# Kernel optimization log

Hardware: AMD Instinct MI355X
Metric: run time of the kernel (lower is better)

The kernel has to match this reference:

```python
import jax, jax.numpy as jnp
import numpy as np
from functools import partial

# norse LIFAdEx default parameters
DT = 0.001
TAU_SYN_INV = 1.0 / 5e-3   # 200.0
TAU_MEM_INV = 1.0 / 1e-2   # 100.0
TAU_ADA_INV = 2.0
ADAPT_CURRENT = 4.0
ADAPT_SPIKE = 0.02
DELTA_T = 0.5
V_LEAK = 0.0
V_TH = 1.0
V_RESET = 0.0
ALPHA = 100.0              # superspike surrogate sharpness
TAU_FILTER_INV = 223.1435511314


@jax.custom_vjp
def superspike(x):
    # forward: heaviside; backward: superspike surrogate grad
    return (x > 0).astype(x.dtype)

def _ss_fwd(x):
    return superspike(x), x

def _ss_bwd(x, g):
    return (g / (ALPHA * jnp.abs(x) + 1.0) ** 2,)

superspike.defvjp(_ss_fwd, _ss_bwd)


def lif_adex_recurrent(x, W_in, W_rec):
    """x: (T,B,F) -> spikes (T,B,H). norse lif_adex_step semantics."""
    T, B, _ = x.shape
    H = W_rec.shape[0]
    # precompute feed-forward input current for all steps: (T,B,H)
    i_in = jnp.einsum('tbf,hf->tbh', x, W_in)

    def step(carry, ic):
        z, v, i, a = carry
        dv = DT * TAU_MEM_INV * ((V_LEAK - v)
                                 + DELTA_T * jnp.exp((v - V_TH) / DELTA_T)
                                 + i - a)
        v_dec = v + dv
        i_dec = i - DT * TAU_SYN_INV * i
        a_dec = a + DT * TAU_ADA_INV * (ADAPT_CURRENT * (v - V_LEAK) - a)
        z_new = superspike(v_dec - V_TH)
        v_new = (1.0 - z_new) * v_dec + z_new * V_RESET
        i_new = i_dec + ic + z @ W_rec.T
        a_new = a_dec + z_new * ADAPT_SPIKE
        return (z_new, v_new, i_new, a_new), z_new

    z0 = jnp.zeros((B, H), x.dtype)
    init = (z0, z0, z0, z0)
    _, spikes = jax.lax.scan(step, init, i_in)
    return spikes


def exp_filter(spikes, W_out, b_out):
    """Linear readout + exponential low-pass filter over time."""
    y = jnp.einsum('tbh,oh->tbo', spikes, W_out) + b_out  # (T,B,O)
    k = DT * TAU_FILTER_INV

    def step(o_prev, y_t):
        o = o_prev + k * (y_t - o_prev)
        return o, o

    o0 = y[0]
    _, rest = jax.lax.scan(step, o0, y[1:])
    return jnp.concatenate([o0[None], rest], axis=0)


def setup_inputs() -> dict:
    key = jax.random.key(0)
    kx, k1, k2, k3, k4 = jax.random.split(key, 5)
    T, B, F, H, O = 500, 128, 128, 512, 32
    x = jax.random.normal(kx, (T, B, F), dtype=jnp.float32)
    W_in = jax.random.normal(k1, (H, F), dtype=jnp.float32) * np.sqrt(2.0 / F)
    W_rec = jax.random.normal(k2, (H, H), dtype=jnp.float32) * np.sqrt(2.0 / H)
    W_out = jax.random.normal(k3, (O, H), dtype=jnp.float32) * np.sqrt(1.0 / H)
    b_out = jax.random.normal(k4, (O,), dtype=jnp.float32) * 0.01
    return {'x': x, 'W_in': W_in, 'W_rec': W_rec, 'W_out': W_out, 'b_out': b_out}


def reference(x, W_in, W_rec, W_out, b_out):
    spikes = lif_adex_recurrent(x, W_in, W_rec)
    return exp_filter(spikes, W_out, b_out)
```

## Files before the change

### kernel.cpp

```cpp
#include <hip/hip_runtime.h>
#include <hip/hip_bf16.h>
#include <cstdint>
#include <cstddef>

#define T_STEPS 500
#define BATCH   128
#define FDIM    128
#define HDIM    512
#define ODIM    32
#define M_ROWS  (T_STEPS * BATCH)
#define ZOFF    (512u << 11)

__device__ __forceinline__ float bfbits2f(unsigned short u) {
    union { unsigned int i; float f; } c; c.i = ((unsigned int)u) << 16; return c.f;
}

__global__ void detect_kernel(const unsigned short* __restrict__ xw, int* __restrict__ flag) {
    __shared__ int cnt;
    if (threadIdx.x == 0) cnt = 0;
    __syncthreads();
    unsigned short w = xw[threadIdx.x * 2];
    int e = (w >> 7) & 0xFF;
    if (e >= 170) atomicAdd(&cnt, 1);
    __syncthreads();
    if (threadIdx.x == 0) *flag = (cnt >= 8) ? 1 : 0;
}

__global__ void prep_kernel(const void* __restrict__ Wrec,
                            const void* __restrict__ Wout,
                            const void* __restrict__ bout,
                            const void* __restrict__ Win,
                            const int* __restrict__ flag,
                            float* __restrict__ WrecT,
                            float* __restrict__ WoutT,
                            float* __restrict__ WinT,
                            float* __restrict__ bout32) {
    const int fp32 = *flag;
    int idx = blockIdx.x * blockDim.x + threadIdx.x;
    if (idx < HDIM * HDIM) {
        int h  = idx / HDIM;
        int hp = idx % HDIM;
        float v = fp32 ? ((const float*)Wrec)[idx]
                       : bfbits2f(((const unsigned short*)Wrec)[idx]);
        WrecT[hp * HDIM + h] = v;
    }
    if (idx < HDIM) WrecT[HDIM * HDIM + idx] = 0.f;
    if (idx < ODIM * HDIM) {
        int o = idx / HDIM;
        int h = idx % HDIM;
        float v = fp32 ? ((const float*)Wout)[idx]
                       : bfbits2f(((const unsigned short*)Wout)[idx]);
        WoutT[h * ODIM + o] = v;
    }
    if (idx < HDIM * FDIM) {
        int h = idx / FDIM;
        int f = idx % FDIM;
        float v = fp32 ? ((const float*)Win)[idx]
                       : bfbits2f(((const unsigned short*)Win)[idx]);
        WinT[f * HDIM + h] = v;
    }
    if (idx < ODIM) {
        bout32[idx] = fp32 ? ((const float*)bout)[idx]
                           : bfbits2f(((const unsigned short*)bout)[idx]);
    }
}

__global__ __launch_bounds__(256) void iin_gemm(const void* __restrict__ x,
                                                const float* __restrict__ WinT,
                                                const int* __restrict__ flag,
                                                float* __restrict__ iin) {
    const int fp32 = *flag;
    const int tid  = threadIdx.x;
    const int m0   = blockIdx.x * 32;

    __shared__ float xs[32][FDIM];

    for (int i = tid; i < 32 * FDIM; i += 256) {
        size_t g = (size_t)m0 * FDIM + i;
        xs[0][i] = fp32 ? ((const float*)x)[g]
                        : bfbits2f(((const unsigned short*)x)[g]);
    }
    __syncthreads();

    float acc[32][2];
#pragma unroll
    for (int m = 0; m < 32; ++m) { acc[m][0] = 0.f; acc[m][1] = 0.f; }

#pragma unroll 4
    for (int k = 0; k < FDIM; ++k) {
        float w0 = WinT[(size_t)k * HDIM + tid];
        float w1 = WinT[(size_t)k * HDIM + 256 + tid];
#pragma unroll
        for (int m = 0; m < 32; ++m) {
            float xv = xs[m][k];
            acc[m][0] += xv * w0;
            acc[m][1] += xv * w1;
        }
    }

#pragma unroll
    for (int m = 0; m < 32; ++m) {
        iin[(size_t)(m0 + m) * HDIM + tid]       = acc[m][0];
        iin[(size_t)(m0 + m) * HDIM + 256 + tid] = acc[m][1];
    }
}

__global__ __launch_bounds__(1024) void scan_kernel(const float* __restrict__ iin,
                                                    const float* __restrict__ WrecT,
                                                    unsigned long long* __restrict__ masksG) {
    const int b    = blockIdx.x;
    const int tid  = threadIdx.x;
    const int h    = tid & (HDIM - 1);
    const int p    = tid >> 9;
    const int lane = tid & 63;
    const int wv   = tid >> 6;

    __shared__ unsigned long long wmask[8];
    __shared__ float part[2][HDIM];
    __shared__ alignas(16) unsigned int slAe[288], slAo[288];
    __shared__ alignas(16) unsigned int slBe[288], slBo[288];
    unsigned int *slOe = slAe, *slOo = slAo;
    unsigned int *slNe = slBe, *slNo = slBo;

    const float kDvC  = 0.1f;
    const float kSyn  = 0.2f;
    const float kAda  = 0.002f;

    float v = 0.f, cur = 0.f, a = 0.f;
    int   cnt = 0;
    const char* WB = (const char*)(WrecT + h);

    for (int t = 0; t < T_STEPS; ++t) {
        float ic = iin[((size_t)t * BATCH + b) * HDIM + h];

        float s = (0.0f - v) + 0.5f * expf((v - 1.0f) * 2.0f);
        s = s + cur;
        s = s - a;
        float v_dec = v + kDvC * s;
        float i_dec = cur - kSyn * cur;
        float a_dec = a + kAda * (4.0f * v - a);
        bool  zk    = (v_dec - 1.0f) > 0.0f;

        unsigned long long m = __ballot(zk);
        if (lane == 0 && wv < 8) {
            wmask[wv] = m;
            masksG[((size_t)t * BATCH + b) * 8 + wv] = m;
        }

        v = zk ? 0.0f : v_dec;
        a = zk ? (a_dec + 0.02f) : a_dec;

        float rsum = 0.f;
        {
            const unsigned int* sl = p ? slOo : slOe;
            const int n  = p ? (cnt >> 1) : ((cnt + 1) >> 1);
            const int ng = (n + 15) >> 4;
            float b0[16], b1[16];
            auto ld16 = [&](int g, float* d) {
                const uint4* q = (const uint4*)(sl + (g << 4));
                uint4 i0 = q[0], i1 = q[1], i2 = q[2], i3 = q[3];
                d[0]  = *(const float*)(WB + i0.x);
                d[1]  = *(const float*)(WB + i0.y);
                d[2]  = *(const float*)(WB + i0.z);
                d[3]  = *(const float*)(WB + i0.w);
                d[4]  = *(const float*)(WB + i1.x);
                d[5]  = *(const float*)(WB + i1.y);
                d[6]  = *(const float*)(WB + i1.z);
                d[7]  = *(const float*)(WB + i1.w);
                d[8]  = *(const float*)(WB + i2.x);
                d[9]  = *(const float*)(WB + i2.y);
                d[10] = *(const float*)(WB + i2.z);
                d[11] = *(const float*)(WB + i2.w);
                d[12] = *(const float*)(WB + i3.x);
                d[13] = *(const float*)(WB + i3.y);
                d[14] = *(const float*)(WB + i3.z);
                d[15] = *(const float*)(WB + i3.w);
            };
            int g = 0;
            if (ng > 0) ld16(0, b0);
            while (g + 2 <= ng) {
                ld16(g + 1, b1);
#pragma unroll
                for (int u = 0; u < 16; ++u) rsum += b0[u];
                if (g + 2 < ng) ld16(g + 2, b0);
#pragma unroll
                for (int u = 0; u < 16; ++u) rsum += b1[u];
                g += 2;
            }
            if (g < ng) {
#pragma unroll
                for (int u = 0; u < 16; ++u) rsum += b0[u];
            }
        }
        part[p][h] = rsum;

        __syncthreads();

        float rec = part[0][h] + part[1][h];
        cur = (i_dec + ic) + rec;

        int total = 0, off = 0;
        const int wv7 = wv & 7;
#pragma unroll
        for (int w = 0; w < 8; ++w) {
            int pc = __popcll(wmask[w]);
            if (w < wv7) off += pc;
            total += pc;
        }
        off += __popcll(m & ((1ull << lane) - 1ull));
        if (zk && p == 0) {
            unsigned int hoff = (unsigned int)h << 11;
            if (off & 1) slNo[off >> 1] = hoff;
            else         slNe[off >> 1] = hoff;
        }
        {
            int ne = (total + 1) >> 1, no = total >> 1;
            int neP = (ne + 15) & ~15, noP = (no + 15) & ~15;
            if (tid < neP - ne) slNe[ne + tid] = ZOFF;
            if (tid < noP - no) slNo[no + tid] = ZOFF;
        }
        cnt = total;

        __syncthreads();

        unsigned int* tp;
        tp = slOe; slOe = slNe; slNe = tp;
        tp = slOo; slOo = slNo; slNo = tp;
    }
}

__global__ __launch_bounds__(256) void y_kernel(const unsigned long long* __restrict__ masks,
                                                const float* __restrict__ WoutT,
                                                const float* __restrict__ bout,
                                                float* __restrict__ y) {
    const int tid = threadIdx.x;
    const int p   = blockIdx.x * 8 + (tid >> 5);
    const int o   = tid & 31;
    const unsigned long long* mp = masks + (size_t)p * 8;
    float acc = 0.f;
#pragma unroll
    for (int w = 0; w < 8; ++w) {
        unsigned long long m = mp[w];
        const float* Wb = WoutT + (size_t)w * 64 * ODIM + o;
        while (m) {
            int j = __builtin_ctzll(m);
            acc += Wb[j * ODIM];
            m &= m - 1;
        }
    }
    y[(size_t)p * ODIM + o] = acc + bout[o];
}

__global__ __launch_bounds__(64) void filter_kernel(const float* __restrict__ y,
                                                    const int* __restrict__ flag,
                                                    void* __restrict__ out) {
    const int p = blockIdx.x * 64 + threadIdx.x;
    const int fp32o = *flag;
    const float kf = 0.2231435511314f;
    float c0[10], c1[10];
#pragma unroll
    for (int u = 0; u < 10; ++u) c0[u] = y[(size_t)u * (BATCH * ODIM) + p];
    float o_state = 0.f;
    for (int base = 0; base < T_STEPS; base += 10) {
        if (base + 10 < T_STEPS) {
#pragma unroll
            for (int u = 0; u < 10; ++u)
                c1[u] = y[(size_t)(base + 10 + u) * (BATCH * ODIM) + p];
        }
#pragma unroll
        for (int u = 0; u < 10; ++u) {
            int t = base + u;
            float yt = c0[u];
            o_state = (t == 0) ? yt : (o_state + kf * (yt - o_state));
            size_t oi = (size_t)t * (BATCH * ODIM) + p;
            if (fp32o) ((float*)out)[oi] = o_state;
            else       ((__hip_bfloat16*)out)[oi] = __float2bfloat16(o_state);
        }
#pragma unroll
        for (int u = 0; u < 10; ++u) c0[u] = c1[u];
    }
}

extern "C" void kernel_launch(void* const* d_in, const int* in_sizes, int n_in,
                              void* d_out, int out_size, void* d_ws, size_t ws_size,
                              hipStream_t stream) {
    const void* x = d_in[0]; const void* Win = d_in[1]; const void* Wrec = d_in[2];
    const void* Wout = d_in[3]; const void* bout = d_in[4];
    for (int i = 0; i < n_in; ++i) {
        switch (in_sizes[i]) {
            case 8192000: x    = d_in[i]; break;
            case 65536:   Win  = d_in[i]; break;
            case 262144:  Wrec = d_in[i]; break;
            case 16384:   Wout = d_in[i]; break;
            case 32:      bout = d_in[i]; break;
            default: break;
        }
    }

    const size_t OFF_FLAG  = 0;
    const size_t OFF_BOUT  = 256;
    const size_t OFF_WOUTT = 512;
    const size_t OFF_WRECT = 66048;
    const size_t OFF_WINT  = 1116672;
    const size_t OFF_MASK  = 1378816;
    const size_t OFF_IIN   = 5474816;
    const size_t OFF_Y     = OFF_IIN;
    const size_t REQUIRED  = OFF_IIN + (size_t)M_ROWS * HDIM * 4;
    if (ws_size < REQUIRED) return;

    char* ws = (char*)d_ws;
    int*    flag   = (int*)(ws + OFF_FLAG);
    float*  bout32 = (float*)(ws + OFF_BOUT);
    float*  WoutT  = (float*)(ws + OFF_WOUTT);
    float*  WrecT  = (float*)(ws + OFF_WRECT);
    float*  WinT   = (float*)(ws + OFF_WINT);
    unsigned long long* masks = (unsigned long long*)(ws + OFF_MASK);
    float*  iin    = (float*)(ws + OFF_IIN);
    float*  y      = (float*)(ws + OFF_Y);

    hipLaunchKernelGGL(detect_kernel, dim3(1), dim3(256), 0, stream,
                       (const unsigned short*)x, flag);
    hipLaunchKernelGGL(prep_kernel, dim3((HDIM * HDIM + 255) / 256), dim3(256), 0, stream,
                       Wrec, Wout, bout, Win, flag, WrecT, WoutT, WinT, bout32);
    hipLaunchKernelGGL(iin_gemm, dim3(M_ROWS / 32), dim3(256), 0, stream,
                       x, WinT, flag, iin);
    hipLaunchKernelGGL(scan_kernel, dim3(BATCH), dim3(1024), 0, stream,
                       iin, WrecT, masks);
    hipLaunchKernelGGL(y_kernel, dim3(M_ROWS / 8), dim3(256), 0, stream,
                       masks, WoutT, bout32, y);
    hipLaunchKernelGGL(filter_kernel, dim3((BATCH * ODIM) / 64), dim3(64), 0, stream,
                       y, flag, d_out);
}
```

Baseline: 995.4 us.

## Repartition recurrent spike gather into 8 slices with float4 weight-row loads

```diff
diff --git a/kernel.cpp b/kernel.cpp
--- a/kernel.cpp
+++ b/kernel.cpp
@@ -110,17 +110,19 @@
                                                     unsigned long long* __restrict__ masksG) {
     const int b    = blockIdx.x;
     const int tid  = threadIdx.x;
-    const int h    = tid & (HDIM - 1);
-    const int p    = tid >> 9;
+    const int q    = tid & 127;
+    const int p    = tid >> 7;
     const int lane = tid & 63;
     const int wv   = tid >> 6;
+    const bool st  = tid < HDIM;
+    const int h    = tid;
 
     __shared__ unsigned long long wmask[8];
-    __shared__ float part[2][HDIM];
-    __shared__ alignas(16) unsigned int slAe[288], slAo[288];
-    __shared__ alignas(16) unsigned int slBe[288], slBo[288];
-    unsigned int *slOe = slAe, *slOo = slAo;
-    unsigned int *slNe = slBe, *slNo = slBo;
+    __shared__ float4 part[8][128];
+    __shared__ alignas(16) unsigned int slA[8][68];
+    __shared__ alignas(16) unsigned int slB[8][68];
+    unsigned int (*slO)[68] = slA;
+    unsigned int (*slN)[68] = slB;
 
     const float kDvC  = 0.1f;
     const float kSyn  = 0.2f;
@@ -128,104 +130,95 @@
 
     float v = 0.f, cur = 0.f, a = 0.f;
     int   cnt = 0;
-    const char* WB = (const char*)(WrecT + h);
+    const char* WQ = (const char*)WrecT + q * 16;
 
     for (int t = 0; t < T_STEPS; ++t) {
-        float ic = iin[((size_t)t * BATCH + b) * HDIM + h];
-
-        float s = (0.0f - v) + 0.5f * expf((v - 1.0f) * 2.0f);
-        s = s + cur;
-        s = s - a;
-        float v_dec = v + kDvC * s;
-        float i_dec = cur - kSyn * cur;
-        float a_dec = a + kAda * (4.0f * v - a);
-        bool  zk    = (v_dec - 1.0f) > 0.0f;
-
-        unsigned long long m = __ballot(zk);
-        if (lane == 0 && wv < 8) {
-            wmask[wv] = m;
-            masksG[((size_t)t * BATCH + b) * 8 + wv] = m;
-        }
-
-        v = zk ? 0.0f : v_dec;
-        a = zk ? (a_dec + 0.02f) : a_dec;
-
-        float rsum = 0.f;
+        float ic = 0.f, i_dec = 0.f;
+        bool  zk = false;
+        unsigned long long m = 0;
+
+        if (st) {
+            ic = iin[((size_t)t * BATCH + b) * HDIM + h];
+            float s = (0.0f - v) + 0.5f * expf((v - 1.0f) * 2.0f);
+            s = s + cur;
+            s = s - a;
+            float v_dec = v + kDvC * s;
+            i_dec = cur - kSyn * cur;
+            float a_dec = a + kAda * (4.0f * v - a);
+            zk = (v_dec - 1.0f) > 0.0f;
+
+            m = __ballot(zk);
+            if (lane == 0) {
+                wmask[wv] = m;
+                masksG[((size_t)t * BATCH + b) * 8 + wv] = m;
+            }
+            v = zk ? 0.0f : v_dec;
+            a = zk ? (a_dec + 0.02f) : a_dec;
+        }
+
+        float4 rs = {0.f, 0.f, 0.f, 0.f};
         {
-            const unsigned int* sl = p ? slOo : slOe;
-            const int n  = p ? (cnt >> 1) : ((cnt + 1) >> 1);
-            const int ng = (n + 15) >> 4;
-            float b0[16], b1[16];
-            auto ld16 = [&](int g, float* d) {
-                const uint4* q = (const uint4*)(sl + (g << 4));
-                uint4 i0 = q[0], i1 = q[1], i2 = q[2], i3 = q[3];
-                d[0]  = *(const float*)(WB + i0.x);
-                d[1]  = *(const float*)(WB + i0.y);
-                d[2]  = *(const float*)(WB + i0.z);
-                d[3]  = *(const float*)(WB + i0.w);
-                d[4]  = *(const float*)(WB + i1.x);
-                d[5]  = *(const float*)(WB + i1.y);
-                d[6]  = *(const float*)(WB + i1.z);
-                d[7]  = *(const float*)(WB + i1.w);
-                d[8]  = *(const float*)(WB + i2.x);
-                d[9]  = *(const float*)(WB + i2.y);
-                d[10] = *(const float*)(WB + i2.z);
-                d[11] = *(const float*)(WB + i2.w);
-                d[12] = *(const float*)(WB + i3.x);
-                d[13] = *(const float*)(WB + i3.y);
-                d[14] = *(const float*)(WB + i3.z);
-                d[15] = *(const float*)(WB + i3.w);
+            const int n  = (cnt + 7 - p) >> 3;
+            const int ng = (n + 3) >> 2;
+            float4 b0[4], b1[4];
+            auto ld4 = [&](int g, float4* d) {
+                uint4 i0 = *(const uint4*)&slO[p][g << 2];
+                d[0] = *(const float4*)(WQ + i0.x);
+                d[1] = *(const float4*)(WQ + i0.y);
+                d[2] = *(const float4*)(WQ + i0.z);
+                d[3] = *(const float4*)(WQ + i0.w);
+            };
+            auto acc4 = [&](const float4* d) {
+#pragma unroll
+                for (int u = 0; u < 4; ++u) {
+                    rs.x += d[u].x; rs.y += d[u].y; rs.z += d[u].z; rs.w += d[u].w;
+                }
             };
             int g = 0;
-            if (ng > 0) ld16(0, b0);
+            if (ng > 0) ld4(0, b0);
             while (g + 2 <= ng) {
-                ld16(g + 1, b1);
-#pragma unroll
-                for (int u = 0; u < 16; ++u) rsum += b0[u];
-                if (g + 2 < ng) ld16(g + 2, b0);
-#pragma unroll
-                for (int u = 0; u < 16; ++u) rsum += b1[u];
+                ld4(g + 1, b1);
+                acc4(b0);
+                if (g + 2 < ng) ld4(g + 2, b0);
+                acc4(b1);
                 g += 2;
             }
-            if (g < ng) {
-#pragma unroll
-                for (int u = 0; u < 16; ++u) rsum += b0[u];
+            if (g < ng) acc4(b0);
+        }
+        part[p][q] = rs;
+
+        __syncthreads();
+
+        int total = 0;
+#pragma unroll
+        for (int w = 0; w < 8; ++w) total += __popcll(wmask[w]);
+
+        if (st) {
+            float rec = 0.f;
+#pragma unroll
+            for (int pp = 0; pp < 8; ++pp)
+                rec += ((const float*)&part[pp][h >> 2])[h & 3];
+            cur = (i_dec + ic) + rec;
+
+            if (zk) {
+                int off = __popcll(m & ((1ull << lane) - 1ull));
+#pragma unroll
+                for (int w = 0; w < 8; ++w)
+                    if (w < wv) off += __popcll(wmask[w]);
+                slN[off & 7][off >> 3] = (unsigned int)h << 11;
             }
-        }
-        part[p][h] = rsum;
+        } else if (tid < HDIM + 32) {
+            int s  = (tid - HDIM) >> 2;
+            int k  = (tid - HDIM) & 3;
+            int ne = (total + 7 - s) >> 3;
+            int padc = (4 - (ne & 3)) & 3;
+            if (k < padc) slN[s][ne + k] = ZOFF;
+        }
+        cnt = total;
 
         __syncthreads();
 
-        float rec = part[0][h] + part[1][h];
-        cur = (i_dec + ic) + rec;
-
-        int total = 0, off = 0;
-        const int wv7 = wv & 7;
-#pragma unroll
-        for (int w = 0; w < 8; ++w) {
-            int pc = __popcll(wmask[w]);
-            if (w < wv7) off += pc;
-            total += pc;
-        }
-        off += __popcll(m & ((1ull << lane) - 1ull));
-        if (zk && p == 0) {
-            unsigned int hoff = (unsigned int)h << 11;
-            if (off & 1) slNo[off >> 1] = hoff;
-            else         slNe[off >> 1] = hoff;
-        }
-        {
-            int ne = (total + 1) >> 1, no = total >> 1;
-            int neP = (ne + 15) & ~15, noP = (no + 15) & ~15;
-            if (tid < neP - ne) slNe[ne + tid] = ZOFF;
-            if (tid < noP - no) slNo[no + tid] = ZOFF;
-        }
-        cnt = total;
-
-        __syncthreads();
-
-        unsigned int* tp;
-        tp = slOe; slOe = slNe; slNe = tp;
-        tp = slOo; slOo = slNo; slNo = tp;
+        unsigned int (*tp)[68] = slO; slO = slN; slN = tp;
     }
 }
 
```

Measured after the change: 906.8 us. 8.9% less time.
